# Kernel tuning notes

Hardware: AMD Instinct MI355X
Metric: run time of the kernel (lower is better)

## Reference

```python
import jax, jax.numpy as jnp
import numpy as np

N_NODES = 100000
N_EDGES = 3200000


def setup_inputs() -> dict:
    key = jax.random.key(0)
    ks = jax.random.split(key, 16)
    inp = {
        "noisy_coords": jax.random.normal(ks[0], (N_NODES, 3), dtype=jnp.float32),
        "atom_types": jax.random.randint(ks[1], (N_NODES,), 0, 2),
        "edge_index": jax.random.randint(ks[2], (2, N_EDGES), 0, N_NODES),
        "emb": jax.random.normal(ks[3], (2, 3), dtype=jnp.float32),
    }
    # GCNConv weights: 6->32->64->64->32->3 (hidden_dim=64)
    dims = [(6, 32), (32, 64), (64, 64), (64, 32), (32, 3)]
    for i, (din, dout) in enumerate(dims, start=1):
        inp[f"W{i}"] = jax.random.normal(ks[3 + i], (din, dout), dtype=jnp.float32) / np.sqrt(din).astype(np.float32)
        inp[f"b{i}"] = jnp.zeros((dout,), dtype=jnp.float32)
    return inp


def _gcn_conv(x, W, b, src, dst, norm, n):
    # GCNConv: X @ W, then symmetric-normalized scatter-add over edges, then bias.
    h = x @ W                       # [N, dout]
    msg = h[src] * norm[:, None]    # gather + edge normalization  [E+N, dout]
    return jax.ops.segment_sum(msg, dst, num_segments=n) + b


def reference(noisy_coords, atom_types, edge_index, emb,
              W1, b1, W2, b2, W3, b3, W4, b4, W5, b5):
    n = noisy_coords.shape[0]
    loop = jnp.arange(n)
    # PyG GCNConv adds self loops and uses deg^{-1/2} (A+I) deg^{-1/2} normalization
    src = jnp.concatenate([edge_index[0], loop])
    dst = jnp.concatenate([edge_index[1], loop])
    deg = jax.ops.segment_sum(jnp.ones(src.shape[0], dtype=jnp.float32), dst, num_segments=n)
    dinv = jnp.where(deg > 0, jax.lax.rsqrt(deg), 0.0)
    norm = dinv[src] * dinv[dst]    # [E+N]

    x = jnp.concatenate([noisy_coords, emb[atom_types]], axis=1)  # [N, 6]
    x = jax.nn.relu(_gcn_conv(x, W1, b1, src, dst, norm, n))
    x = jax.nn.relu(_gcn_conv(x, W2, b2, src, dst, norm, n))
    x = jax.nn.relu(_gcn_conv(x, W3, b3, src, dst, norm, n))
    x = jax.nn.relu(_gcn_conv(x, W4, b4, src, dst, norm, n))
    x = _gcn_conv(x, W5, b5, src, dst, norm, n)  # final layer: no relu
    return x
```

## Files before the change

kernel.cpp:

```cpp
#include <hip/hip_runtime.h>
#include <hip/hip_fp16.h>

#define NBLK_BIN 256
#define NBKT 196
#define BWIN 512
#define CAP 128


typedef unsigned int uint;

union U32H2 { uint u; __half2 h; };

__device__ inline float2 h2_to_f2(uint u) {
    U32H2 c; c.u = u;
    return __half22float2(c.h);
}
__device__ inline uint f2_to_h2(float a, float b) {
    U32H2 c; c.h = __floats2half2_rn(a, b);
    return c.u;
}

__global__ __launch_bounds__(1024) void bin_kernel(const int* __restrict__ src,
                                                   const int* __restrict__ dst,
                                                   int2* __restrict__ pairs,
                                                   int* __restrict__ blkcnt, int e) {
    __shared__ int lcnt[NBKT];
    int blk = blockIdx.x, tid = threadIdx.x;
    for (int t = tid; t < NBKT; t += 1024) lcnt[t] = 0;
    __syncthreads();
    int chunk = (e + NBLK_BIN - 1) / NBLK_BIN;
    int base = blk * chunk;
    int end = min(e, base + chunk);
    for (int i = base + tid; i < end; i += 1024) {
        int s = src[i], d = dst[i];
        int b = d >> 9;
        int pos = atomicAdd(&lcnt[b], 1);
        if (pos < CAP) pairs[((size_t)blk * NBKT + b) * CAP + pos] = make_int2(s, d);
    }
    __syncthreads();
    for (int t = tid; t < NBKT; t += 1024) blkcnt[blk * NBKT + t] = min(lcnt[t], CAP);
}

__global__ __launch_bounds__(1024) void fill_kernel(const int2* __restrict__ pairs,
                                                    const int* __restrict__ blkcnt,
                                                    int* __restrict__ srcs,
                                                    int* __restrict__ cnt,
                                                    int* __restrict__ rowptr,
                                                    float* __restrict__ dinv, int n) {
    __shared__ int lc[BWIN];
    __shared__ int ps[BWIN];
    __shared__ int sm[NBLK_BIN];
    __shared__ int gbase_s;
    int b = blockIdx.x, tid = threadIdx.x;
    int nbase = b << 9;
    if (tid < BWIN) lc[tid] = 0;
    for (int t = tid; t < NBLK_BIN; t += 1024) sm[t] = blkcnt[t * NBKT + b];
    if (tid == 0) gbase_s = 0;
    __syncthreads();
    {
        long long tot = (long long)NBLK_BIN * b;
        int lsum = 0;
        for (long long j = tid; j < tot; j += 1024) {
            int blk = (int)(j / b);
            int bp  = (int)(j - (long long)blk * b);
            lsum += blkcnt[blk * NBKT + bp];
        }
        for (int o = 32; o > 0; o >>= 1) lsum += __shfl_down(lsum, o, 64);
        if ((tid & 63) == 0 && lsum != 0) atomicAdd(&gbase_s, lsum);
    }
    int wave = tid >> 6, lane = tid & 63;
    for (int blk = wave; blk < NBLK_BIN; blk += 16) {
        int m = sm[blk];
        const int2* p = pairs + ((size_t)blk * NBKT + b) * CAP;
        for (int i = lane; i < m; i += 64) atomicAdd(&lc[p[i].y - nbase], 1);
    }
    __syncthreads();
    int myc = (tid < BWIN) ? lc[tid] : 0;
    if (tid < BWIN) ps[tid] = myc;
    __syncthreads();
    for (int off = 1; off < BWIN; off <<= 1) {
        int t = 0;
        if (tid < BWIN && tid >= off) t = ps[tid - off];
        __syncthreads();
        if (tid < BWIN) ps[tid] += t;
        __syncthreads();
    }
    int gbase = gbase_s;
    if (tid < BWIN) {
        int ex = ps[tid] - myc;
        int vtx = nbase + tid;
        if (vtx < n) {
            cnt[vtx] = myc;
            rowptr[vtx] = gbase + ex;
            dinv[vtx] = rsqrtf(1.0f + (float)myc);
        }
    }
    __syncthreads();
    if (tid < BWIN) lc[tid] = ps[tid] - myc;
    __syncthreads();
    for (int blk = wave; blk < NBLK_BIN; blk += 16) {
        int m = sm[blk];
        const int2* p = pairs + ((size_t)blk * NBKT + b) * CAP;
        for (int i = lane; i < m; i += 64) {
            int2 e2 = p[i];
            int o = atomicAdd(&lc[e2.y - nbase], 1);
            srcs[gbase + o] = e2.x;
        }
    }
}


__global__ __launch_bounds__(256) void build_x0_h_kernel(const float* __restrict__ coords,
                                                         const int* __restrict__ at,
                                                         const float* __restrict__ emb,
                                                         const float* __restrict__ dinv,
                                                         uint* __restrict__ x, int n) {
    int v = blockIdx.x * 256 + threadIdx.x;
    if (v >= n) return;
    float dv = dinv[v];
    float c0 = coords[3 * v + 0] * dv;
    float c1 = coords[3 * v + 1] * dv;
    float c2 = coords[3 * v + 2] * dv;
    int t = at[v];
    float e0 = emb[3 * t + 0] * dv;
    float e1 = emb[3 * t + 1] * dv;
    float e2 = emb[3 * t + 2] * dv;
    uint* row = x + (size_t)v * 4;
    row[0] = f2_to_h2(c0, c1);
    row[1] = f2_to_h2(c2, e0);
    row[2] = f2_to_h2(e1, e2);
    row[3] = 0;
}

template <int TPN, bool HAS_BIAS, bool RELU>
__global__ __launch_bounds__(256) void agg_v4_kernel(const uint* __restrict__ in_,
                                                     const float* __restrict__ dinv,
                                                     const int* __restrict__ rowptr,
                                                     const int* __restrict__ cnt,
                                                     const int* __restrict__ srcs,
                                                     const float* __restrict__ bias,
                                                     uint* __restrict__ out_, int n) {
    const uint4* in = (const uint4*)in_;
    uint4* out = (uint4*)out_;
    int gid = blockIdx.x * 256 + threadIdx.x;
    int v = gid / TPN, q = gid % TPN;
    if (v >= n) return;
    float ax[4], ay[4];
    {
        uint4 s0 = in[(size_t)v * TPN + q];
        uint su[4] = {s0.x, s0.y, s0.z, s0.w};
#pragma unroll
        for (int u = 0; u < 4; ++u) { float2 f = h2_to_f2(su[u]); ax[u] = f.x; ay[u] = f.y; }
    }
    int start = rowptr[v];
    int len = cnt[v];
    int k = 0;
    for (; k + 4 <= len; k += 4) {
        int sA = srcs[start + k];
        int sB = srcs[start + k + 1];
        int sC = srcs[start + k + 2];
        int sD = srcs[start + k + 3];
        uint4 fA = in[(size_t)sA * TPN + q];
        uint4 fB = in[(size_t)sB * TPN + q];
        uint4 fC = in[(size_t)sC * TPN + q];
        uint4 fD = in[(size_t)sD * TPN + q];
        uint ua[4] = {fA.x, fA.y, fA.z, fA.w};
        uint ub[4] = {fB.x, fB.y, fB.z, fB.w};
        uint uc[4] = {fC.x, fC.y, fC.z, fC.w};
        uint ud[4] = {fD.x, fD.y, fD.z, fD.w};
#pragma unroll
        for (int u = 0; u < 4; ++u) {
            float2 a = h2_to_f2(ua[u]);
            float2 b = h2_to_f2(ub[u]);
            float2 c = h2_to_f2(uc[u]);
            float2 d = h2_to_f2(ud[u]);
            ax[u] += (a.x + b.x) + (c.x + d.x);
            ay[u] += (a.y + b.y) + (c.y + d.y);
        }
    }
    for (; k < len; ++k) {
        int s = srcs[start + k];
        uint4 f = in[(size_t)s * TPN + q];
        uint uu[4] = {f.x, f.y, f.z, f.w};
#pragma unroll
        for (int u = 0; u < 4; ++u) { float2 t = h2_to_f2(uu[u]); ax[u] += t.x; ay[u] += t.y; }
    }
    float dv = dinv[v];
#pragma unroll
    for (int u = 0; u < 4; ++u) {
        ax[u] *= dv; ay[u] *= dv;
        if (HAS_BIAS) { ax[u] += bias[8 * q + 2 * u]; ay[u] += bias[8 * q + 2 * u + 1]; }
        if (RELU) { ax[u] = fmaxf(ax[u], 0.0f); ay[u] = fmaxf(ay[u], 0.0f); }
    }
    uint4 o;
    o.x = f2_to_h2(ax[0], ay[0]);
    o.y = f2_to_h2(ax[1], ay[1]);
    o.z = f2_to_h2(ax[2], ay[2]);
    o.w = f2_to_h2(ax[3], ay[3]);
    out[(size_t)v * TPN + q] = o;
}

__global__ __launch_bounds__(256) void agg_l4l5_kernel(const uint* __restrict__ in_,
                                                       const float* __restrict__ dinv,
                                                       const int* __restrict__ rowptr,
                                                       const int* __restrict__ cnt,
                                                       const int* __restrict__ srcs,
                                                       const float* __restrict__ b4,
                                                       const float* __restrict__ W5,
                                                       float* __restrict__ outf, int n) {
    const uint4* in = (const uint4*)in_;
    int gid = blockIdx.x * 256 + threadIdx.x;
    int v = gid >> 2, q = gid & 3;
    if (v >= n) return;
    float ax[4], ay[4];
    {
        uint4 s0 = in[(size_t)v * 4 + q];
        uint su[4] = {s0.x, s0.y, s0.z, s0.w};
#pragma unroll
        for (int u = 0; u < 4; ++u) { float2 f = h2_to_f2(su[u]); ax[u] = f.x; ay[u] = f.y; }
    }
    int start = rowptr[v];
    int len = cnt[v];
    int k = 0;
    for (; k + 4 <= len; k += 4) {
        int sA = srcs[start + k];
        int sB = srcs[start + k + 1];
        int sC = srcs[start + k + 2];
        int sD = srcs[start + k + 3];
        uint4 fA = in[(size_t)sA * 4 + q];
        uint4 fB = in[(size_t)sB * 4 + q];
        uint4 fC = in[(size_t)sC * 4 + q];
        uint4 fD = in[(size_t)sD * 4 + q];
        uint ua[4] = {fA.x, fA.y, fA.z, fA.w};
        uint ub[4] = {fB.x, fB.y, fB.z, fB.w};
        uint uc[4] = {fC.x, fC.y, fC.z, fC.w};
        uint ud[4] = {fD.x, fD.y, fD.z, fD.w};
#pragma unroll
        for (int u = 0; u < 4; ++u) {
            float2 a = h2_to_f2(ua[u]);
            float2 b = h2_to_f2(ub[u]);
            float2 c = h2_to_f2(uc[u]);
            float2 d = h2_to_f2(ud[u]);
            ax[u] += (a.x + b.x) + (c.x + d.x);
            ay[u] += (a.y + b.y) + (c.y + d.y);
        }
    }
    for (; k < len; ++k) {
        int s = srcs[start + k];
        uint4 f = in[(size_t)s * 4 + q];
        uint uu[4] = {f.x, f.y, f.z, f.w};
#pragma unroll
        for (int u = 0; u < 4; ++u) { float2 t = h2_to_f2(uu[u]); ax[u] += t.x; ay[u] += t.y; }
    }
    float dv = dinv[v];
    float feat[8];
#pragma unroll
    for (int u = 0; u < 4; ++u) {
        float fx = ax[u] * dv + b4[8 * q + 2 * u];
        float fy = ay[u] * dv + b4[8 * q + 2 * u + 1];
        feat[2 * u]     = fmaxf(fx, 0.0f);
        feat[2 * u + 1] = fmaxf(fy, 0.0f);
    }
    float p0 = 0.f, p1 = 0.f, p2 = 0.f;
#pragma unroll
    for (int m = 0; m < 8; ++m) {
        int j = 8 * q + m;
        p0 = fmaf(feat[m], W5[j * 3 + 0], p0);
        p1 = fmaf(feat[m], W5[j * 3 + 1], p1);
        p2 = fmaf(feat[m], W5[j * 3 + 2], p2);
    }
#pragma unroll
    for (int m = 1; m < 4; m <<= 1) {
        p0 += __shfl_xor(p0, m, 4);
        p1 += __shfl_xor(p1, m, 4);
        p2 += __shfl_xor(p2, m, 4);
    }
    float o = (q == 0) ? p0 : (q == 1 ? p1 : (q == 2 ? p2 : 0.0f));
    outf[(size_t)v * 4 + q] = (q < 3) ? o * dv : 0.0f;
}

template <int DIN, int DOUT, int DOUTH2, bool HAS_BIAS, bool RELU, bool SCALE>
__global__ __launch_bounds__(256) void gemm_h_kernel(const uint* __restrict__ xin,
                                                     const float* __restrict__ W,
                                                     const float* __restrict__ bias,
                                                     const float* __restrict__ dinv,
                                                     uint* __restrict__ xout,
                                                     int istride_u, int ostride, int n) {
    __shared__ float wlds[DIN * DOUT];
    for (int i = threadIdx.x; i < DIN * DOUT; i += 256) wlds[i] = W[i];
    __syncthreads();
    int gid = blockIdx.x * 256 + threadIdx.x;
    int v = gid / DOUTH2, j2 = gid % DOUTH2;
    if (v >= n) return;
    int j1 = 2 * j2;
    const uint* xr = xin + (size_t)v * istride_u;
    float acc0 = 0.0f, acc1 = 0.0f;
#pragma unroll
    for (int ku = 0; ku < DIN / 2; ++ku) {
        float2 xf = h2_to_f2(xr[ku]);
        int k = 2 * ku;
        acc0 = fmaf(xf.x, wlds[k * DOUT + j1], acc0);
        acc0 = fmaf(xf.y, wlds[(k + 1) * DOUT + j1], acc0);
        if (j1 + 1 < DOUT) {
            acc1 = fmaf(xf.x, wlds[k * DOUT + j1 + 1], acc1);
            acc1 = fmaf(xf.y, wlds[(k + 1) * DOUT + j1 + 1], acc1);
        }
    }
    if (HAS_BIAS) {
        acc0 += bias[j1];
        if (j1 + 1 < DOUT) acc1 += bias[j1 + 1];
    }
    if (RELU) { acc0 = fmaxf(acc0, 0.0f); acc1 = fmaxf(acc1, 0.0f); }
    if (SCALE) { float dv = dinv[v]; acc0 *= dv; acc1 *= dv; }
    xout[(size_t)v * ostride + j2] = f2_to_h2(acc0, acc1);
}

#define G34_NODES 16
__global__ __launch_bounds__(256) void gemm34_kernel(const uint* __restrict__ xin,
                                                     const float* __restrict__ W3,
                                                     const float* __restrict__ b3,
                                                     const float* __restrict__ W4,
                                                     const float* __restrict__ dinv,
                                                     uint* __restrict__ xout,
                                                     int n) {
    __shared__ float w3[64 * 64];
    __shared__ float w4[64 * 32];
    __shared__ float hb[G34_NODES][65];
    for (int i = threadIdx.x; i < 64 * 64; i += 256) w3[i] = W3[i];
    for (int i = threadIdx.x; i < 64 * 32; i += 256) w4[i] = W4[i];
    __syncthreads();
    int i  = threadIdx.x >> 4;
    int j2 = threadIdx.x & 15;
    int v  = blockIdx.x * G34_NODES + i;
    bool ok = (v < n);
    int j1 = 2 * j2;
    float a0 = 0.f, a1 = 0.f, a2 = 0.f, a3 = 0.f;
    if (ok) {
        const uint* xr = xin + (size_t)v * 32;
#pragma unroll
        for (int ku = 0; ku < 32; ++ku) {
            float2 xf = h2_to_f2(xr[ku]);
            int k = 2 * ku;
            a0 = fmaf(xf.x, w3[k * 64 + j1],      a0);
            a0 = fmaf(xf.y, w3[(k + 1) * 64 + j1],      a0);
            a1 = fmaf(xf.x, w3[k * 64 + j1 + 1],  a1);
            a1 = fmaf(xf.y, w3[(k + 1) * 64 + j1 + 1],  a1);
            a2 = fmaf(xf.x, w3[k * 64 + j1 + 32], a2);
            a2 = fmaf(xf.y, w3[(k + 1) * 64 + j1 + 32], a2);
            a3 = fmaf(xf.x, w3[k * 64 + j1 + 33], a3);
            a3 = fmaf(xf.y, w3[(k + 1) * 64 + j1 + 33], a3);
        }
        hb[i][j1]      = fmaxf(a0 + b3[j1],      0.f);
        hb[i][j1 + 1]  = fmaxf(a1 + b3[j1 + 1],  0.f);
        hb[i][j1 + 32] = fmaxf(a2 + b3[j1 + 32], 0.f);
        hb[i][j1 + 33] = fmaxf(a3 + b3[j1 + 33], 0.f);
    }
    __syncthreads();
    float c0 = 0.f, c1 = 0.f;
#pragma unroll
    for (int k = 0; k < 64; ++k) {
        float hk = hb[i][k];
        c0 = fmaf(hk, w4[k * 32 + j1],     c0);
        c1 = fmaf(hk, w4[k * 32 + j1 + 1], c1);
    }
    if (ok) {
        float dv = dinv[v];
        xout[(size_t)v * 16 + j2] = f2_to_h2(c0 * dv, c1 * dv);
    }
}

__global__ __launch_bounds__(256) void agg_f4_kernel(const float* __restrict__ in_,
                                                     const float* __restrict__ dinv,
                                                     const int* __restrict__ rowptr,
                                                     const int* __restrict__ cnt,
                                                     const int* __restrict__ srcs,
                                                     const float* __restrict__ b,
                                                     float* __restrict__ out, int n) {
    const float4* in = (const float4*)in_;
    int v = blockIdx.x * 256 + threadIdx.x;
    if (v >= n) return;
    float4 s = in[v];
    float a0 = s.x, a1 = s.y, a2 = s.z;
    int start = rowptr[v];
    int len = cnt[v];
    int k = 0;
    for (; k + 4 <= len; k += 4) {
        int sA = srcs[start + k];
        int sB = srcs[start + k + 1];
        int sC = srcs[start + k + 2];
        int sD = srcs[start + k + 3];
        float4 fA = in[sA];
        float4 fB = in[sB];
        float4 fC = in[sC];
        float4 fD = in[sD];
        a0 += (fA.x + fB.x) + (fC.x + fD.x);
        a1 += (fA.y + fB.y) + (fC.y + fD.y);
        a2 += (fA.z + fB.z) + (fC.z + fD.z);
    }
    for (; k < len; ++k) {
        float4 f = in[srcs[start + k]];
        a0 += f.x; a1 += f.y; a2 += f.z;
    }
    float dv = dinv[v];
    out[(size_t)v * 3 + 0] = a0 * dv + b[0];
    out[(size_t)v * 3 + 1] = a1 * dv + b[1];
    out[(size_t)v * 3 + 2] = a2 * dv + b[2];
}


extern "C" void kernel_launch(void* const* d_in, const int* in_sizes, int n_in,
                              void* d_out, int out_size, void* d_ws, size_t ws_size,
                              hipStream_t stream) {
    const float* coords = (const float*)d_in[0];
    const int* at       = (const int*)d_in[1];
    const int* ei       = (const int*)d_in[2];
    const float* emb    = (const float*)d_in[3];
    const float* W1 = (const float*)d_in[4];  const float* b1 = (const float*)d_in[5];
    const float* W2 = (const float*)d_in[6];  const float* b2 = (const float*)d_in[7];
    const float* W3 = (const float*)d_in[8];  const float* b3 = (const float*)d_in[9];
    const float* W4 = (const float*)d_in[10]; const float* b4 = (const float*)d_in[11];
    const float* W5 = (const float*)d_in[12]; const float* b5 = (const float*)d_in[13];
    float* out = (float*)d_out;

    const int n = in_sizes[0] / 3;
    const int e = in_sizes[2] / 2;
    const int* src = ei;
    const int* dst = ei + e;

    char* ws = (char*)d_ws;
    size_t off = 0;
    float* dinv   = (float*)(ws + off); off += (size_t)n * 4;
    int*   cnt    = (int*)(ws + off);   off += (size_t)n * 4;
    int*   rowptr = (int*)(ws + off);   off += (size_t)n * 4;
    int*   blkcnt = (int*)(ws + off);   off += (size_t)NBLK_BIN * NBKT * 4;
    int*   srcs   = (int*)(ws + off);   off += (size_t)e * 4;
    char*  alias  = ws + off;
    int2*  pairs  = (int2*)alias;
    uint*  A_h    = (uint*)alias;
    uint*  B_h    = A_h + (size_t)n * 32;
    float* B_f    = (float*)(B_h + (size_t)n * 32);

    int nb = (n + 255) / 256;

    bin_kernel<<<NBLK_BIN, 1024, 0, stream>>>(src, dst, pairs, blkcnt, e);
    fill_kernel<<<NBKT, 1024, 0, stream>>>(pairs, blkcnt, srcs, cnt, rowptr, dinv, n);

    build_x0_h_kernel<<<nb, 256, 0, stream>>>(coords, at, emb, dinv, A_h, n);

    auto blocks = [](long long threads) { return (int)((threads + 255) / 256); };

    agg_v4_kernel<1, false, false><<<blocks((long long)n), 256, 0, stream>>>(
        A_h, dinv, rowptr, cnt, srcs, nullptr, B_h, n);
    gemm_h_kernel<6, 32, 16, true, true, true><<<blocks((long long)n * 16), 256, 0, stream>>>(
        B_h, W1, b1, dinv, A_h, 4, 16, n);

    agg_v4_kernel<4, false, false><<<blocks((long long)n * 4), 256, 0, stream>>>(
        A_h, dinv, rowptr, cnt, srcs, nullptr, B_h, n);
    gemm_h_kernel<32, 64, 32, true, true, true><<<blocks((long long)n * 32), 256, 0, stream>>>(
        B_h, W2, b2, dinv, A_h, 16, 32, n);

    agg_v4_kernel<8, false, false><<<blocks((long long)n * 8), 256, 0, stream>>>(
        A_h, dinv, rowptr, cnt, srcs, nullptr, B_h, n);
    gemm34_kernel<<<(n + G34_NODES - 1) / G34_NODES, 256, 0, stream>>>(
        B_h, W3, b3, W4, dinv, A_h, n);

    agg_l4l5_kernel<<<blocks((long long)n * 4), 256, 0, stream>>>(
        A_h, dinv, rowptr, cnt, srcs, b4, W5, B_f, n);

    agg_f4_kernel<<<blocks((long long)n), 256, 0, stream>>>(
        B_f, dinv, rowptr, cnt, srcs, b5, out, n);
}
```

Measured before the change: 426.1 us.

## Register-tile fused layer 3/4 GEMM over 64 nodes per block with swizzled LDS

Rewrites the fused W3/W4 transform so each block handles 64 nodes instead of 16. Each thread computes a 4x4 register tile in the first GEMM and 4x2 in the second. Weights are repacked into float4 chunks along K, and inputs are read as uint4 vectors, so each weight read from LDS is reused across four nodes. The hidden buffer uses an XOR swizzle to avoid bank conflicts. The goal is to cut LDS traffic and the weight reload per block, at the cost of more registers and fewer blocks.

Result: no change. 431.2 us (+1.2%).

```diff
diff --git a/kernel.cpp b/kernel.cpp
--- a/kernel.cpp
+++ b/kernel.cpp
@@ -315,7 +315,6 @@
     xout[(size_t)v * ostride + j2] = f2_to_h2(acc0, acc1);
 }
 
-#define G34_NODES 16
 __global__ __launch_bounds__(256) void gemm34_kernel(const uint* __restrict__ xin,
                                                      const float* __restrict__ W3,
                                                      const float* __restrict__ b3,
@@ -323,49 +322,109 @@
                                                      const float* __restrict__ dinv,
                                                      uint* __restrict__ xout,
                                                      int n) {
-    __shared__ float w3[64 * 64];
-    __shared__ float w4[64 * 32];
-    __shared__ float hb[G34_NODES][65];
-    for (int i = threadIdx.x; i < 64 * 64; i += 256) w3[i] = W3[i];
-    for (int i = threadIdx.x; i < 64 * 32; i += 256) w4[i] = W4[i];
-    __syncthreads();
-    int i  = threadIdx.x >> 4;
+    __shared__ float4 w3c[16][64];
+    __shared__ float4 w4c[16][32];
+    __shared__ float4 hb4[64][16];
+    for (int idx = threadIdx.x; idx < 16 * 64; idx += 256) {
+        int kc = idx >> 6, c = idx & 63;
+        w3c[kc][c] = make_float4(W3[(4 * kc + 0) * 64 + c], W3[(4 * kc + 1) * 64 + c],
+                                 W3[(4 * kc + 2) * 64 + c], W3[(4 * kc + 3) * 64 + c]);
+    }
+    for (int idx = threadIdx.x; idx < 16 * 32; idx += 256) {
+        int kc = idx >> 5, c = idx & 31;
+        w4c[kc][c] = make_float4(W4[(4 * kc + 0) * 32 + c], W4[(4 * kc + 1) * 32 + c],
+                                 W4[(4 * kc + 2) * 32 + c], W4[(4 * kc + 3) * 32 + c]);
+    }
+    __syncthreads();
+    int r  = threadIdx.x >> 4;
     int j2 = threadIdx.x & 15;
-    int v  = blockIdx.x * G34_NODES + i;
-    bool ok = (v < n);
-    int j1 = 2 * j2;
-    float a0 = 0.f, a1 = 0.f, a2 = 0.f, a3 = 0.f;
-    if (ok) {
-        const uint* xr = xin + (size_t)v * 32;
-#pragma unroll
-        for (int ku = 0; ku < 32; ++ku) {
-            float2 xf = h2_to_f2(xr[ku]);
-            int k = 2 * ku;
-            a0 = fmaf(xf.x, w3[k * 64 + j1],      a0);
-            a0 = fmaf(xf.y, w3[(k + 1) * 64 + j1],      a0);
-            a1 = fmaf(xf.x, w3[k * 64 + j1 + 1],  a1);
-            a1 = fmaf(xf.y, w3[(k + 1) * 64 + j1 + 1],  a1);
-            a2 = fmaf(xf.x, w3[k * 64 + j1 + 32], a2);
-            a2 = fmaf(xf.y, w3[(k + 1) * 64 + j1 + 32], a2);
-            a3 = fmaf(xf.x, w3[k * 64 + j1 + 33], a3);
-            a3 = fmaf(xf.y, w3[(k + 1) * 64 + j1 + 33], a3);
-        }
-        hb[i][j1]      = fmaxf(a0 + b3[j1],      0.f);
-        hb[i][j1 + 1]  = fmaxf(a1 + b3[j1 + 1],  0.f);
-        hb[i][j1 + 32] = fmaxf(a2 + b3[j1 + 32], 0.f);
-        hb[i][j1 + 33] = fmaxf(a3 + b3[j1 + 33], 0.f);
-    }
-    __syncthreads();
-    float c0 = 0.f, c1 = 0.f;
-#pragma unroll
-    for (int k = 0; k < 64; ++k) {
-        float hk = hb[i][k];
-        c0 = fmaf(hk, w4[k * 32 + j1],     c0);
-        c1 = fmaf(hk, w4[k * 32 + j1 + 1], c1);
-    }
-    if (ok) {
-        float dv = dinv[v];
-        xout[(size_t)v * 16 + j2] = f2_to_h2(c0 * dv, c1 * dv);
+    int vbase = blockIdx.x * 64;
+    int li[4]; int vv[4]; bool ok[4];
+#pragma unroll
+    for (int t = 0; t < 4; ++t) { li[t] = r + 16 * t; vv[t] = vbase + li[t]; ok[t] = vv[t] < n; }
+
+    float acc[4][4];
+#pragma unroll
+    for (int t = 0; t < 4; ++t)
+#pragma unroll
+        for (int u = 0; u < 4; ++u) acc[t][u] = 0.0f;
+
+    for (int kb = 0; kb < 8; ++kb) {
+        uint4 xa[4];
+#pragma unroll
+        for (int t = 0; t < 4; ++t)
+            xa[t] = ok[t] ? ((const uint4*)(xin + (size_t)vv[t] * 32))[kb]
+                          : make_uint4(0u, 0u, 0u, 0u);
+        float xf[4][8];
+#pragma unroll
+        for (int t = 0; t < 4; ++t) {
+            float2 f0 = h2_to_f2(xa[t].x);
+            float2 f1 = h2_to_f2(xa[t].y);
+            float2 f2 = h2_to_f2(xa[t].z);
+            float2 f3 = h2_to_f2(xa[t].w);
+            xf[t][0] = f0.x; xf[t][1] = f0.y;
+            xf[t][2] = f1.x; xf[t][3] = f1.y;
+            xf[t][4] = f2.x; xf[t][5] = f2.y;
+            xf[t][6] = f3.x; xf[t][7] = f3.y;
+        }
+#pragma unroll
+        for (int u = 0; u < 4; ++u) {
+            int c = j2 + 16 * u;
+            float4 wa = w3c[2 * kb][c];
+            float4 wb = w3c[2 * kb + 1][c];
+#pragma unroll
+            for (int t = 0; t < 4; ++t) {
+                acc[t][u] = fmaf(xf[t][0], wa.x, acc[t][u]);
+                acc[t][u] = fmaf(xf[t][1], wa.y, acc[t][u]);
+                acc[t][u] = fmaf(xf[t][2], wa.z, acc[t][u]);
+                acc[t][u] = fmaf(xf[t][3], wa.w, acc[t][u]);
+                acc[t][u] = fmaf(xf[t][4], wb.x, acc[t][u]);
+                acc[t][u] = fmaf(xf[t][5], wb.y, acc[t][u]);
+                acc[t][u] = fmaf(xf[t][6], wb.z, acc[t][u]);
+                acc[t][u] = fmaf(xf[t][7], wb.w, acc[t][u]);
+            }
+        }
+    }
+#pragma unroll
+    for (int u = 0; u < 4; ++u) {
+        int c = j2 + 16 * u;
+        float bc = b3[c];
+#pragma unroll
+        for (int t = 0; t < 4; ++t) {
+            float h = fmaxf(acc[t][u] + bc, 0.0f);
+            int pos = (c >> 2) ^ (li[t] & 7);
+            ((float*)hb4)[li[t] * 64 + pos * 4 + (c & 3)] = h;
+        }
+    }
+    __syncthreads();
+
+    float acc2[4][2];
+#pragma unroll
+    for (int t = 0; t < 4; ++t) { acc2[t][0] = 0.0f; acc2[t][1] = 0.0f; }
+    for (int kc = 0; kc < 16; ++kc) {
+        float4 wlo = w4c[kc][j2];
+        float4 whi = w4c[kc][j2 + 16];
+#pragma unroll
+        for (int t = 0; t < 4; ++t) {
+            float4 h4 = hb4[li[t]][kc ^ (li[t] & 7)];
+            acc2[t][0] = fmaf(h4.x, wlo.x, acc2[t][0]);
+            acc2[t][0] = fmaf(h4.y, wlo.y, acc2[t][0]);
+            acc2[t][0] = fmaf(h4.z, wlo.z, acc2[t][0]);
+            acc2[t][0] = fmaf(h4.w, wlo.w, acc2[t][0]);
+            acc2[t][1] = fmaf(h4.x, whi.x, acc2[t][1]);
+            acc2[t][1] = fmaf(h4.y, whi.y, acc2[t][1]);
+            acc2[t][1] = fmaf(h4.z, whi.z, acc2[t][1]);
+            acc2[t][1] = fmaf(h4.w, whi.w, acc2[t][1]);
+        }
+    }
+#pragma unroll
+    for (int t = 0; t < 4; ++t) {
+        if (ok[t]) {
+            float dv = dinv[vv[t]];
+            __half* o = (__half*)(xout + (size_t)vv[t] * 16);
+            o[j2]      = __float2half(acc2[t][0] * dv);
+            o[j2 + 16] = __float2half(acc2[t][1] * dv);
+        }
     }
 }
 
@@ -461,7 +520,7 @@
 
     agg_v4_kernel<8, false, false><<<blocks((long long)n * 8), 256, 0, stream>>>(
         A_h, dinv, rowptr, cnt, srcs, nullptr, B_h, n);
-    gemm34_kernel<<<(n + G34_NODES - 1) / G34_NODES, 256, 0, stream>>>(
+    gemm34_kernel<<<(n + 63) / 64, 256, 0, stream>>>(
         B_h, W3, b3, W4, dinv, A_h, n);
 
     agg_l4l5_kernel<<<blocks((long long)n * 4), 256, 0, stream>>>(
```
